# Kernel optimization log

Hardware: AMD Instinct MI355X
Metric: run time of the kernel (lower is better)

Reference implementation:

```python
import jax, jax.numpy as jnp
import numpy as np

L, D, H, N, R = 4, 256, 512, 16, 8  # layers, d_model, hidden=2*d_model, state_dim, dt_rank
OUT_LEN, IN_DIM = 96, 32
EPS = 1e-5


def _layernorm(v, g, b):
    m = jnp.mean(v, axis=-1, keepdims=True)
    var = jnp.mean((v - m) ** 2, axis=-1, keepdims=True)
    return (v - m) / jnp.sqrt(var + EPS) * g + b


def _pos_encoding(T, d):
    pos = jnp.arange(T, dtype=jnp.float32)[:, None]
    div = jnp.exp(jnp.arange(0, d, 2, dtype=jnp.float32) * (-np.log(10000.0) / d))
    pe = jnp.zeros((T, d), dtype=jnp.float32)
    pe = pe.at[:, 0::2].set(jnp.sin(pos * div))
    pe = pe.at[:, 1::2].set(jnp.cos(pos * div))
    return pe


def setup_inputs() -> dict:
    key = jax.random.key(0)
    ks = jax.random.split(key, 20)
    inp = {
        "x": jax.random.normal(ks[0], (8, 1024, IN_DIM), dtype=jnp.float32),
        "emb_w": jax.random.normal(ks[1], (D, IN_DIM), dtype=jnp.float32) * 0.1,
        "emb_b": jnp.zeros((D,), dtype=jnp.float32),
        "norm_g": jnp.ones((L, D), dtype=jnp.float32),
        "norm_b": jnp.zeros((L, D), dtype=jnp.float32),
        "in_w": jax.random.normal(ks[2], (L, H, D), dtype=jnp.float32) * (1.0 / np.sqrt(D)),
        "conv_w": jax.random.normal(ks[3], (L, H, 1, 3), dtype=jnp.float32) * 0.5,
        "A_p": jax.random.normal(ks[4], (L, H, N), dtype=jnp.float32) * 0.01,
        "D_p": jnp.ones((L, H), dtype=jnp.float32),
        "dt1_w": jax.random.normal(ks[5], (L, R, H), dtype=jnp.float32) * (1.0 / np.sqrt(H)),
        "dt1_b": jnp.zeros((L, R), dtype=jnp.float32),
        "dt2_w": jax.random.normal(ks[6], (L, H, R), dtype=jnp.float32) * (1.0 / np.sqrt(R)),
        "dt2_b": jnp.zeros((L, H), dtype=jnp.float32),
        "out_w": jax.random.normal(ks[7], (L, D, H), dtype=jnp.float32) * (1.0 / np.sqrt(H)),
        "final_g": jnp.ones((D,), dtype=jnp.float32),
        "final_b": jnp.zeros((D,), dtype=jnp.float32),
        "head1_w": jax.random.normal(ks[8], (D, D), dtype=jnp.float32) * (1.0 / np.sqrt(D)),
        "head1_b": jnp.zeros((D,), dtype=jnp.float32),
        "head2_w": jax.random.normal(ks[9], (OUT_LEN, D), dtype=jnp.float32) * (1.0 / np.sqrt(D)),
        "head2_b": jnp.zeros((OUT_LEN,), dtype=jnp.float32),
    }
    return inp


def _mamba_block(h, g, b, in_w, conv_w, A_p, D_p, dt1_w, dt1_b, dt2_w, dt2_b, out_w):
    res = h
    v = _layernorm(h, g, b)            # [B,T,D]
    v = jnp.einsum('btd,hd->bth', v, in_w)  # [B,T,H]
    # depthwise conv1d, kernel 3, padding 1, groups=H
    vc = jnp.transpose(v, (0, 2, 1))   # [B,H,T]
    vc = jax.lax.conv_general_dilated(vc, conv_w, window_strides=(1,),
                                      padding=[(1, 1)], feature_group_count=H,
                                      dimension_numbers=('NCH', 'OIH', 'NCH'))
    v = jnp.transpose(jax.nn.silu(vc), (0, 2, 1))  # [B,T,H]
    dt = jax.nn.relu(jnp.einsum('bth,rh->btr', v, dt1_w) + dt1_b)
    dt = jnp.einsum('btr,hr->bth', dt, dt2_w) + dt2_b
    dt = jax.nn.softplus(dt)           # [B,T,H]
    A = -jnp.exp(A_p)                  # [H,N]
    safe_A = jnp.where(jnp.abs(A) < 1e-5, jnp.ones_like(A), A)

    B_sz = v.shape[0]
    state0 = jnp.zeros((B_sz, H, N), dtype=v.dtype)

    def step(state, inp):
        x_t, dt_t = inp  # [B,H] each
        dA = A * dt_t[..., None]            # [B,H,N]
        discA = jnp.exp(dA)
        discB = (discA - 1.0) / safe_A * dt_t[..., None]
        state = discA * state + discB * x_t[..., None]
        y = jnp.einsum('bhn,hn->bh', state, A_p) + D_p * x_t
        return state, y

    xs = (jnp.transpose(v, (1, 0, 2)), jnp.transpose(dt, (1, 0, 2)))  # [T,B,H]
    _, ys = jax.lax.scan(step, state0, xs)
    y = jnp.transpose(ys, (1, 0, 2))   # [B,T,H]
    return res + jnp.einsum('bth,dh->btd', y, out_w)


def reference(x, emb_w, emb_b, norm_g, norm_b, in_w, conv_w, A_p, D_p,
              dt1_w, dt1_b, dt2_w, dt2_b, out_w, final_g, final_b,
              head1_w, head1_b, head2_w, head2_b):
    h = jnp.einsum('bti,di->btd', x, emb_w) + emb_b  # [B,T,D]
    h = h + _pos_encoding(h.shape[1], D)[None]
    for l in range(L):
        h = _mamba_block(h, norm_g[l], norm_b[l], in_w[l], conv_w[l], A_p[l],
                         D_p[l], dt1_w[l], dt1_b[l], dt2_w[l], dt2_b[l], out_w[l])
    h = _layernorm(h, final_g, final_b)
    h = h[:, -1, :]                    # last token [B,D]
    h = jax.nn.silu(h @ head1_w.T + head1_b)
    return h @ head2_w.T + head2_b     # [B, OUT_LEN]
```

## Files before the change

kernel.cpp:

```cpp
#include <hip/hip_runtime.h>
#include <hip/hip_bf16.h>
#include <math.h>

#define BB 8
#define TT 1024
#define DD 256
#define HH 512
#define NN 16
#define RR 8
#define OUT_LEN 96
#define IN_DIM 32
#define MM (BB*TT)

#define SC 16
#define CC (TT/SC)

typedef unsigned short u16;
typedef unsigned int u32;
typedef __attribute__((ext_vector_type(8))) short short8;
typedef __attribute__((ext_vector_type(8))) unsigned short u16x8;
typedef __attribute__((ext_vector_type(4))) float float4v;

__device__ __forceinline__ u16 f2bf(float f) {
    __hip_bfloat16 h = __float2bfloat16(f);
    return *(u16*)&h;
}
__device__ __forceinline__ float bf2f(u16 u) {
    u32 v = ((u32)u) << 16;
    return *(float*)&v;
}

#define GLD_LDS16(src, dst) __builtin_amdgcn_global_load_lds( \
    (const __attribute__((address_space(1))) void*)(src),     \
    (__attribute__((address_space(3))) void*)(dst), 16, 0, 0)

#define SBAR()   asm volatile("s_barrier" ::: "memory")
#define VMCNT0() asm volatile("s_waitcnt vmcnt(0)" ::: "memory")
#define VMCNT4() asm volatile("s_waitcnt vmcnt(4)" ::: "memory")
#define VMCNT6() asm volatile("s_waitcnt vmcnt(6)" ::: "memory")
#define VMCNT8() asm volatile("s_waitcnt vmcnt(8)" ::: "memory")

__global__ __launch_bounds__(256) void embed_ln_cvt_kernel(
    const float* __restrict__ x, const float* __restrict__ emb_w,
    const float* __restrict__ emb_b,
    const float* __restrict__ g, const float* __restrict__ b,
    float* __restrict__ h, u16* __restrict__ lnout,
    const float* __restrict__ w_in, u16* __restrict__ wbf_in,
    const float* __restrict__ w_out, u16* __restrict__ wbf_out, int nw)
{
    int bid = blockIdx.x;
    if (bid >= MM) {
        int i = (bid - MM) * 256 + threadIdx.x;
        if (i < nw) wbf_in[i] = f2bf(w_in[i]);
        else        wbf_out[i - nw] = f2bf(w_out[i - nw]);
        return;
    }

    int bt = bid;
    int d  = threadIdx.x;
    int t  = bt & (TT - 1);

    __shared__ float xs[IN_DIM];
    __shared__ float red[4], red2[4];
    if (threadIdx.x < IN_DIM) xs[threadIdx.x] = x[bt * IN_DIM + threadIdx.x];
    __syncthreads();

    const float* w = emb_w + d * IN_DIM;
    float acc = emb_b[d];
#pragma unroll
    for (int i = 0; i < IN_DIM; i++) acc = fmaf(xs[i], w[i], acc);

    int i2 = d & ~1;
    float div = __expf(-(float)i2 * 0.0359778918f);
    float arg = (float)t * div;
    float pe = (d & 1) ? __cosf(arg) : __sinf(arg);
    float val = acc + pe;
    h[bt * DD + d] = val;

    float s = val;
#pragma unroll
    for (int o = 32; o > 0; o >>= 1) s += __shfl_down(s, o);
    int lane = d & 63, wave = d >> 6;
    if (lane == 0) red[wave] = s;
    __syncthreads();
    float mean = (red[0] + red[1] + red[2] + red[3]) * (1.0f / DD);

    float c = val - mean;
    float s2 = c * c;
#pragma unroll
    for (int o = 32; o > 0; o >>= 1) s2 += __shfl_down(s2, o);
    if (lane == 0) red2[wave] = s2;
    __syncthreads();
    float var = (red2[0] + red2[1] + red2[2] + red2[3]) * (1.0f / DD);

    lnout[bt * DD + d] = f2bf(c * rsqrtf(var + 1e-5f) * g[d] + b[d]);
}

template<int BM, int BN, int OUT_BF16>
__global__ __launch_bounds__(256) void gemm_bf16(
    const u16* __restrict__ A, const u16* __restrict__ B,
    void* __restrict__ Cv, int M, int N, int K, int addC)
{
    constexpr int BK = 64;
    constexpr int MT = BM / 32;
    constexpr int NT = BN / 32;
    static_assert(BM == 128 && BN == 64, "vmcnt count assumes 6 loads/thread");

    __shared__ __align__(16) u16 Al[2][8][BM][8];
    __shared__ __align__(16) u16 Bl[2][8][BN][8];

    const int tid = threadIdx.x;
    const int bm = blockIdx.y * BM;
    const int bn = blockIdx.x * BN;
    const int wid = tid >> 6, lane = tid & 63;
    const int wm = wid >> 1, wn = wid & 1;
    const int lq = lane >> 4, lm = lane & 15;

    float4v acc[MT][NT];
#pragma unroll
    for (int i = 0; i < MT; i++)
#pragma unroll
        for (int j = 0; j < NT; j++) acc[i][j] = (float4v){0.f, 0.f, 0.f, 0.f};

#pragma unroll
    for (int it = 0; it < (8 * BM) / 256; it++) {
        int c = it * 256 + tid;
        int q = c / BM, row = c % BM;
        GLD_LDS16(A + (size_t)(bm + row) * K + q * 8, &Al[0][q][row][0]);
    }
#pragma unroll
    for (int it = 0; it < (8 * BN) / 256; it++) {
        int c = it * 256 + tid;
        int q = c / BN, row = c % BN;
        GLD_LDS16(B + (size_t)(bn + row) * K + q * 8, &Bl[0][q][row][0]);
    }

    const int nt = K / BK;
    int cur = 0;
    for (int i = 0; i < nt; i++) {
        if (i + 1 < nt) {
            int nxt = cur ^ 1;
            int k1 = (i + 1) * BK;
#pragma unroll
            for (int it = 0; it < (8 * BM) / 256; it++) {
                int c = it * 256 + tid;
                int q = c / BM, row = c % BM;
                GLD_LDS16(A + (size_t)(bm + row) * K + k1 + q * 8, &Al[nxt][q][row][0]);
            }
#pragma unroll
            for (int it = 0; it < (8 * BN) / 256; it++) {
                int c = it * 256 + tid;
                int q = c / BN, row = c % BN;
                GLD_LDS16(B + (size_t)(bn + row) * K + k1 + q * 8, &Bl[nxt][q][row][0]);
            }
            VMCNT6();
        } else {
            VMCNT0();
        }
        SBAR();

        short8 af[2][MT], bf[2][NT];
#pragma unroll
        for (int kk = 0; kk < 2; kk++) {
#pragma unroll
            for (int mt = 0; mt < MT; mt++)
                af[kk][mt] = *(const short8*)&Al[cur][kk * 4 + lq][wm * (BM / 2) + mt * 16 + lm][0];
#pragma unroll
            for (int nt2 = 0; nt2 < NT; nt2++)
                bf[kk][nt2] = *(const short8*)&Bl[cur][kk * 4 + lq][wn * (BN / 2) + nt2 * 16 + lm][0];
        }

#pragma unroll
        for (int kk = 0; kk < 2; kk++)
#pragma unroll
            for (int mt = 0; mt < MT; mt++)
#pragma unroll
                for (int nt2 = 0; nt2 < NT; nt2++)
                    acc[mt][nt2] = __builtin_amdgcn_mfma_f32_16x16x32_bf16(
                        af[kk][mt], bf[kk][nt2], acc[mt][nt2], 0, 0, 0);
        SBAR();
        cur ^= 1;
    }

#pragma unroll
    for (int mt = 0; mt < MT; mt++)
#pragma unroll
        for (int nt2 = 0; nt2 < NT; nt2++) {
            int row0 = bm + wm * (BM / 2) + mt * 16 + lq * 4;
            int col  = bn + wn * (BN / 2) + nt2 * 16 + lm;
#pragma unroll
            for (int r = 0; r < 4; r++) {
                float vv = acc[mt][nt2][r];
                if (OUT_BF16) {
                    ((u16*)Cv)[(size_t)(row0 + r) * N + col] = f2bf(vv);
                } else {
                    float* cp = (float*)Cv + (size_t)(row0 + r) * N + col;
                    if (addC) vv += *cp;
                    *cp = vv;
                }
            }
        }
}

__device__ __forceinline__ float softplus_f(float s) {
    return (s > 20.0f) ? s : __logf(1.0f + __expf(s));
}

__global__ __launch_bounds__(512, 4) void conv_scan1(
    const u16* __restrict__ vbf, const float* __restrict__ cwg,
    const float* __restrict__ w1g, const float* __restrict__ b1g,
    const float* __restrict__ dt2_w, const float* __restrict__ dt2_b,
    const float* __restrict__ A_p,
    u16* __restrict__ vsb, float* __restrict__ dtr,
    u16* __restrict__ Lst, float* __restrict__ sdt)
{
    const int c = blockIdx.x;
    const int b = blockIdx.y;
    const int tid = threadIdx.x;
    const int wave = tid >> 6, lane = tid & 63;
    const int h0 = lane * 8;

    __shared__ float w1s[RR * 2 * 256];
    __shared__ u16   a_lds[SC][HH];
    __shared__ float ds[SC * RR];

#pragma unroll
    for (int i = 0; i < 2; i++) {
        int rci = wave + i * 8;
        int r = rci >> 1, jc = rci & 1;
        float4 wv = *(const float4*)(w1g + r * HH + lane * 8 + jc * 4);
        *(float4*)&w1s[rci * 256 + lane * 4] = wv;
    }
    __syncthreads();

    const float* wp = cwg + h0 * 3;
#pragma unroll
    for (int i = 0; i < 2; i++) {
        int tr = wave + i * 8;
        int t  = c * SC + tr;
        size_t m = (size_t)b * TT + t;

        const u16* vrow = vbf + m * HH + h0;
        u16x8 x0 = *(const u16x8*)vrow;
        u16x8 xm = (t > 0)      ? *(const u16x8*)(vrow - HH) : (u16x8)(0);
        u16x8 xp = (t < TT - 1) ? *(const u16x8*)(vrow + HH) : (u16x8)(0);

        float a[8];
        u16x8 o;
#pragma unroll
        for (int j = 0; j < 8; j++) {
            float s = wp[j * 3] * bf2f(xm[j]);
            s = fmaf(wp[j * 3 + 1], bf2f(x0[j]), s);
            s = fmaf(wp[j * 3 + 2], bf2f(xp[j]), s);
            s = s / (1.0f + __expf(-s));
            a[j] = s;
            o[j] = f2bf(s);
        }
        *(u16x8*)(vsb + m * HH + h0) = o;
        *(u16x8*)&a_lds[tr][h0]      = o;

        float acc[RR];
#pragma unroll
        for (int r = 0; r < RR; r++) {
            float4 wlo = *(const float4*)&w1s[(r * 2 + 0) * 256 + lane * 4];
            float4 whi = *(const float4*)&w1s[(r * 2 + 1) * 256 + lane * 4];
            float s = a[0] * wlo.x;
            s = fmaf(a[1], wlo.y, s);
            s = fmaf(a[2], wlo.z, s);
            s = fmaf(a[3], wlo.w, s);
            s = fmaf(a[4], whi.x, s);
            s = fmaf(a[5], whi.y, s);
            s = fmaf(a[6], whi.z, s);
            s = fmaf(a[7], whi.w, s);
            acc[r] = s;
        }
#pragma unroll
        for (int r = 0; r < RR; r++) {
#pragma unroll
            for (int o2 = 1; o2 < 64; o2 <<= 1) acc[r] += __shfl_xor(acc[r], o2);
        }
        if (lane == 0) {
#pragma unroll
            for (int r = 0; r < RR; r++) acc[r] = fmaxf(acc[r] + b1g[r], 0.0f);
            *(float4*)(dtr + m * RR)     = make_float4(acc[0], acc[1], acc[2], acc[3]);
            *(float4*)(dtr + m * RR + 4) = make_float4(acc[4], acc[5], acc[6], acc[7]);
#pragma unroll
            for (int r = 0; r < RR; r++) ds[tr * RR + r] = acc[r];
        }
    }
    __syncthreads();

    const int h = tid;
    float A2[NN], invA[NN], st[NN];
    const float* ap = A_p + h * NN;
#pragma unroll
    for (int n = 0; n < NN; n++) {
        float av = -__expf(ap[n]);
        A2[n] = av * 1.44269504f;
        invA[n] = 1.0f / av;
        st[n] = 0.0f;
    }
    float w2[RR];
#pragma unroll
    for (int r = 0; r < RR; r++) w2[r] = dt2_w[h * RR + r];
    float b2 = dt2_b[h];

    float xv = bf2f(a_lds[0][h]);
    float s_dt = 0.0f;
#pragma unroll 2
    for (int t = 0; t < SC; t++) {
        float xn = (t + 1 < SC) ? bf2f(a_lds[t + 1][h]) : 0.0f;
        float s = b2;
#pragma unroll
        for (int r = 0; r < RR; r++) s = fmaf(ds[t * RR + r], w2[r], s);
        float dt = softplus_f(s);
        s_dt += dt;
        float dtx = dt * xv;
#pragma unroll
        for (int n = 0; n < NN; n++) {
            float e = __builtin_amdgcn_exp2f(A2[n] * dt);
            float u = invA[n] * dtx;
            st[n] = fmaf(e, st[n] + u, -u);
        }
        xv = xn;
    }

    size_t base = (((size_t)c * BB + b) * HH + h) * NN;
    u16x8 lo, hi;
#pragma unroll
    for (int n = 0; n < 8; n++) { lo[n] = f2bf(st[n]); hi[n] = f2bf(st[n + 8]); }
    *(u16x8*)(Lst + base)     = lo;
    *(u16x8*)(Lst + base + 8) = hi;
    sdt[((size_t)c * BB + b) * HH + h] = s_dt;
}

__global__ __launch_bounds__(256) void scan_carry_par(
    const float* __restrict__ A_p, const float* __restrict__ sdt,
    u16* __restrict__ Lst)
{
    int gw   = (blockIdx.x << 2) | (threadIdx.x >> 6);
    int lane = threadIdx.x & 63;
    int b = gw >> 9;
    int h = gw & 511;

    size_t sidx = ((size_t)lane * BB + b) * HH + h;
    float sd = sdt[sidx];
    const float* ap = A_p + h * NN;
    u16x8 Llo = *(const u16x8*)(Lst + sidx * NN);
    u16x8 Lhi = *(const u16x8*)(Lst + sidx * NN + 8);
    u16x8 Elo, Ehi;
#pragma unroll
    for (int n = 0; n < NN; n++) {
        float An = -__expf(ap[n]);
        float p  = __expf(An * sd);
        float lv = bf2f((n < 8) ? Llo[n] : Lhi[n - 8]);
#pragma unroll
        for (int d2 = 1; d2 < 64; d2 <<= 1) {
            float pp = __shfl_up(p, d2);
            float pl = __shfl_up(lv, d2);
            if (lane >= d2) { lv = fmaf(pl, p, lv); p = pp * p; }
        }
        float E = __shfl_up(lv, 1);
        if (lane == 0) E = 0.0f;
        if (n < 8) Elo[n] = f2bf(E); else Ehi[n - 8] = f2bf(E);
    }
    *(u16x8*)(Lst + sidx * NN)     = Elo;
    *(u16x8*)(Lst + sidx * NN + 8) = Ehi;
}

__global__ __launch_bounds__(512) void scan2_gemm2_ln(
    const u16* __restrict__ vsb, const float* __restrict__ dtr,
    const float* __restrict__ dt2_w, const float* __restrict__ dt2_b,
    const float* __restrict__ A_p, const float* __restrict__ D_p,
    const u16* __restrict__ carry,
    const u16* __restrict__ B,
    float* __restrict__ h,
    const float* __restrict__ g, const float* __restrict__ bb,
    u16* __restrict__ lnout, int doLN,
    const float* __restrict__ w1h, const float* __restrict__ b1h,
    const float* __restrict__ w2h, const float* __restrict__ b2h,
    float* __restrict__ outp, int doHead)
{
    const int bid = blockIdx.x;
    const int b   = bid >> 5;
    const int tb  = bid & 31;
    const int t0  = tb * 32;
    const int c0  = tb * 2;
    const int bm  = bid * 32;

    const int tid = threadIdx.x;
    const int wid = tid >> 6;
    const int lane = tid & 63;
    const int lq = lane >> 4, lm = lane & 15;
    const int wm = wid >> 2;
    const int wn = wid & 3;

    __shared__ __align__(16) u16 Yl[32 * 512];
    __shared__ __align__(16) u16 Bl[3][8][256][8];
    __shared__ float ds[32 * RR];
    __shared__ float rs[4][32], qs[4][32];
    __shared__ float hn[DD], sl1[DD];

#pragma unroll
    for (int pt = 0; pt < 2; pt++) {
#pragma unroll
        for (int it = 0; it < 4; it++) {
            int cth = it * 512 + tid;
            int q = cth >> 8, row = cth & 255;
            GLD_LDS16(B + (size_t)row * 512 + pt * 64 + q * 8, &Bl[pt][q][row][0]);
        }
    }

    if (tid < 256) {
        int tr = tid >> 3, r = tid & 7;
        ds[tid] = dtr[((size_t)b * TT + t0 + tr) * RR + r];
    }

    const int hh = tid;
    float A2[NN], invA[NN], Ap[NN], w2[RR];
    const float* ap = A_p + hh * NN;
#pragma unroll
    for (int n = 0; n < NN; n++) {
        float apv = ap[n]; Ap[n] = apv;
        float a = -__expf(apv);
        A2[n] = a * 1.44269504f; invA[n] = 1.0f / a;
    }
#pragma unroll
    for (int r = 0; r < RR; r++) w2[r] = dt2_w[hh * RR + r];
    float b2 = dt2_b[hh];
    float Dp = D_p[hh];
    __syncthreads();

#pragma unroll
    for (int cc = 0; cc < 2; cc++) {
        int cg = c0 + cc;
        float st[NN];
        size_t cbase = (((size_t)cg * BB + b) * HH + hh) * NN;
        u16x8 clo = *(const u16x8*)(carry + cbase);
        u16x8 chi = *(const u16x8*)(carry + cbase + 8);
#pragma unroll
        for (int n = 0; n < 8; n++) { st[n] = bf2f(clo[n]); st[n + 8] = bf2f(chi[n]); }

        const u16* vbase = vsb + ((size_t)b * TT + (size_t)cg * SC) * HH + hh;
        float xv = bf2f(vbase[0]);
#pragma unroll 2
        for (int t = 0; t < SC; t++) {
            float xn = (t + 1 < SC) ? bf2f(vbase[(size_t)(t + 1) * HH]) : 0.0f;
            int tr = cc * SC + t;
            float s = b2;
#pragma unroll
            for (int r = 0; r < RR; r++) s = fmaf(ds[tr * RR + r], w2[r], s);
            float dt = softplus_f(s);
            float dtx = dt * xv;
            float acc = Dp * xv;
#pragma unroll
            for (int n = 0; n < NN; n++) {
                float e = __builtin_amdgcn_exp2f(A2[n] * dt);
                float u = invA[n] * dtx;
                st[n] = fmaf(e, st[n] + u, -u);
                acc = fmaf(st[n], Ap[n], acc);
            }
            Yl[tr * 512 + (hh ^ ((tr & 7) << 3))] = f2bf(acc);
            xv = xn;
        }
    }
    __syncthreads();

    float4v acc4[4];
#pragma unroll
    for (int j = 0; j < 4; j++) acc4[j] = (float4v){0.f, 0.f, 0.f, 0.f};

    for (int i = 0; i < 8; i++) {
        if (i + 2 < 8) {
            int nb = (i + 2) % 3;
            int k1 = (i + 2) * 64;
#pragma unroll
            for (int it = 0; it < 4; it++) {
                int cth = it * 512 + tid;
                int q = cth >> 8, row = cth & 255;
                GLD_LDS16(B + (size_t)row * 512 + k1 + q * 8, &Bl[nb][q][row][0]);
            }
            VMCNT8();
        } else if (i + 1 < 8) {
            VMCNT4();
        } else {
            VMCNT0();
        }
        SBAR();

        int cur = i % 3;
        int k0 = i * 64;
        short8 af[2], bf[2][4];
#pragma unroll
        for (int kk = 0; kk < 2; kk++) {
            int row = wm * 16 + lm;
            int kg  = (k0 >> 3) + kk * 4 + lq;
            af[kk] = *(const short8*)&Yl[row * 512 + ((kg ^ (row & 7)) << 3)];
#pragma unroll
            for (int nt = 0; nt < 4; nt++)
                bf[kk][nt] = *(const short8*)&Bl[cur][kk * 4 + lq][wn * 64 + nt * 16 + lm][0];
        }
#pragma unroll
        for (int kk = 0; kk < 2; kk++)
#pragma unroll
            for (int nt = 0; nt < 4; nt++)
                acc4[nt] = __builtin_amdgcn_mfma_f32_16x16x32_bf16(
                    af[kk], bf[kk][nt], acc4[nt], 0, 0, 0);
        SBAR();
    }

    float val[4][4];
    float s1[4] = {0.f, 0.f, 0.f, 0.f}, s2[4] = {0.f, 0.f, 0.f, 0.f};
#pragma unroll
    for (int r = 0; r < 4; r++) {
        int row = bm + wm * 16 + lq * 4 + r;
#pragma unroll
        for (int nt = 0; nt < 4; nt++) {
            int col = wn * 64 + nt * 16 + lm;
            float v = acc4[nt][r] + h[(size_t)row * DD + col];
            val[r][nt] = v;
            s1[r] += v;
            s2[r] = fmaf(v, v, s2[r]);
            h[(size_t)row * DD + col] = v;
        }
    }
#pragma unroll
    for (int r = 0; r < 4; r++) {
#pragma unroll
        for (int o = 1; o < 16; o <<= 1) {
            s1[r] += __shfl_xor(s1[r], o);
            s2[r] += __shfl_xor(s2[r], o);
        }
    }
    if (lm == 0) {
#pragma unroll
        for (int r = 0; r < 4; r++) {
            rs[wn][wm * 16 + lq * 4 + r] = s1[r];
            qs[wn][wm * 16 + lq * 4 + r] = s2[r];
        }
    }
    __syncthreads();

    if (doLN) {
#pragma unroll
        for (int r = 0; r < 4; r++) {
            int i = wm * 16 + lq * 4 + r;
            int row = bm + i;
            float mean = (rs[0][i] + rs[1][i] + rs[2][i] + rs[3][i]) * (1.0f / DD);
            float var  = (qs[0][i] + qs[1][i] + qs[2][i] + qs[3][i]) * (1.0f / DD) - mean * mean;
            float rstd = rsqrtf(var + 1e-5f);
#pragma unroll
            for (int nt = 0; nt < 4; nt++) {
                int col = wn * 64 + nt * 16 + lm;
                lnout[(size_t)row * DD + col] =
                    f2bf((val[r][nt] - mean) * rstd * g[col] + bb[col]);
            }
        }
    }

    if (doHead && tb == 31) {
        const int i31 = 31;
        float mean = (rs[0][i31] + rs[1][i31] + rs[2][i31] + rs[3][i31]) * (1.0f / DD);
        float var  = (qs[0][i31] + qs[1][i31] + qs[2][i31] + qs[3][i31]) * (1.0f / DD) - mean * mean;
        float rstd = rsqrtf(var + 1e-5f);
        const size_t row = (size_t)bm + 31;

        if (tid < DD) {
            float v = h[row * DD + tid];
            hn[tid] = (v - mean) * rstd * g[tid] + bb[tid];
        }
        __syncthreads();

        if (tid < DD) {
            float a1 = b1h[tid];
            const float* w1r = w1h + tid * DD;
#pragma unroll 8
            for (int k = 0; k < DD; k++) a1 = fmaf(hn[k], w1r[k], a1);
            sl1[tid] = a1 / (1.0f + __expf(-a1));
        }
        __syncthreads();

        if (tid < OUT_LEN) {
            float a2 = b2h[tid];
            const float* w2r = w2h + tid * DD;
#pragma unroll 8
            for (int k = 0; k < DD; k++) a2 = fmaf(sl1[k], w2r[k], a2);
            outp[b * OUT_LEN + tid] = a2;
        }
    }
}

extern "C" void kernel_launch(void* const* d_in, const int* in_sizes, int n_in,
                              void* d_out, int out_size, void* d_ws, size_t ws_size,
                              hipStream_t stream)
{
    (void)in_sizes; (void)n_in; (void)out_size; (void)ws_size;

    const float* x       = (const float*)d_in[0];
    const float* emb_w   = (const float*)d_in[1];
    const float* emb_b   = (const float*)d_in[2];
    const float* norm_g  = (const float*)d_in[3];
    const float* norm_b  = (const float*)d_in[4];
    const float* in_w    = (const float*)d_in[5];
    const float* conv_w  = (const float*)d_in[6];
    const float* A_p     = (const float*)d_in[7];
    const float* D_p     = (const float*)d_in[8];
    const float* dt1_w   = (const float*)d_in[9];
    const float* dt1_b   = (const float*)d_in[10];
    const float* dt2_w   = (const float*)d_in[11];
    const float* dt2_b   = (const float*)d_in[12];
    const float* out_w   = (const float*)d_in[13];
    const float* final_g = (const float*)d_in[14];
    const float* final_b = (const float*)d_in[15];
    const float* head1_w = (const float*)d_in[16];
    const float* head1_b = (const float*)d_in[17];
    const float* head2_w = (const float*)d_in[18];
    const float* head2_b = (const float*)d_in[19];
    float* outp = (float*)d_out;

    char* ws = (char*)d_ws;
    float* h     = (float*)ws;                ws += (size_t)MM * DD * 4;
    u16*   vbf   = (u16*)ws;                  ws += (size_t)MM * HH * 2;
    u16*   vsb   = (u16*)ws;                  ws += (size_t)MM * HH * 2;
    u16*   lnbuf = (u16*)ws;                  ws += (size_t)MM * DD * 2;
    float* dtr   = (float*)ws;                ws += (size_t)MM * RR * 4;
    u16*   Lst   = (u16*)ws;                  ws += (size_t)CC * BB * HH * NN * 2;
    float* sdt   = (float*)ws;                ws += (size_t)CC * BB * HH * 4;
    u16*   wbf_in  = (u16*)ws;                ws += (size_t)4 * HH * DD * 2;
    u16*   wbf_out = (u16*)ws;                ws += (size_t)4 * DD * HH * 2;

    const int NW = 4 * HH * DD;
    embed_ln_cvt_kernel<<<MM + (2 * NW) / 256, 256, 0, stream>>>(
        x, emb_w, emb_b, norm_g, norm_b, h, lnbuf,
        in_w, wbf_in, out_w, wbf_out, NW);

    for (int l = 0; l < 4; l++) {
        gemm_bf16<128, 64, 1><<<dim3(HH / 64, MM / 128), 256, 0, stream>>>(
            lnbuf, wbf_in + (size_t)l * HH * DD, vbf, MM, HH, DD, 0);

        conv_scan1<<<dim3(CC, BB), 512, 0, stream>>>(
            vbf, conv_w + (size_t)l * HH * 3,
            dt1_w + (size_t)l * RR * HH, dt1_b + l * RR,
            dt2_w + (size_t)l * HH * RR, dt2_b + l * HH,
            A_p + (size_t)l * HH * NN,
            vsb, dtr, Lst, sdt);

        scan_carry_par<<<(BB * HH) / 4, 256, 0, stream>>>(
            A_p + (size_t)l * HH * NN, sdt, Lst);

        const float* g_next = (l < 3) ? (norm_g + (l + 1) * DD) : final_g;
        const float* b_next = (l < 3) ? (norm_b + (l + 1) * DD) : final_b;
        scan2_gemm2_ln<<<MM / 32, 512, 0, stream>>>(
            vsb, dtr, dt2_w + (size_t)l * HH * RR, dt2_b + l * HH,
            A_p + (size_t)l * HH * NN, D_p + l * HH,
            Lst, wbf_out + (size_t)l * DD * HH,
            h, g_next, b_next, lnbuf, (l < 3) ? 1 : 0,
            head1_w, head1_b, head2_w, head2_b, outp, (l == 3) ? 1 : 0);
    }
}
```

Before: 467.9 us.

## Halve scan2_gemm2_ln tile to one chunk per block and double-buffer B

Each scan2_gemm2_ln block now handles one 16-step scan chunk (16 rows) instead of two. The grid doubles to 512 blocks and each thread scans only 16 timesteps, which shortens the serial scan per block and adds more blocks to fill the GPU. The output GEMM uses 8 waves each owning 32 columns, with a K=32 double-buffered B pipeline and launch_bounds(512,4) to allow higher occupancy. In exchange, the whole out_w weight matrix is streamed into LDS twice as many times across the grid, and the per-step barriers double.

Measured after the change: 479.1 us. +2.4%, slower.

```diff
diff --git a/kernel.cpp b/kernel.cpp
--- a/kernel.cpp
+++ b/kernel.cpp
@@ -36,9 +36,8 @@
 
 #define SBAR()   asm volatile("s_barrier" ::: "memory")
 #define VMCNT0() asm volatile("s_waitcnt vmcnt(0)" ::: "memory")
-#define VMCNT4() asm volatile("s_waitcnt vmcnt(4)" ::: "memory")
+#define VMCNT2() asm volatile("s_waitcnt vmcnt(2)" ::: "memory")
 #define VMCNT6() asm volatile("s_waitcnt vmcnt(6)" ::: "memory")
-#define VMCNT8() asm volatile("s_waitcnt vmcnt(8)" ::: "memory")
 
 __global__ __launch_bounds__(256) void embed_ln_cvt_kernel(
     const float* __restrict__ x, const float* __restrict__ emb_w,
@@ -368,7 +367,7 @@
     *(u16x8*)(Lst + sidx * NN + 8) = Ehi;
 }
 
-__global__ __launch_bounds__(512) void scan2_gemm2_ln(
+__global__ __launch_bounds__(512, 4) void scan2_gemm2_ln(
     const u16* __restrict__ vsb, const float* __restrict__ dtr,
     const float* __restrict__ dt2_w, const float* __restrict__ dt2_b,
     const float* __restrict__ A_p, const float* __restrict__ D_p,
@@ -382,41 +381,45 @@
     float* __restrict__ outp, int doHead)
 {
     const int bid = blockIdx.x;
-    const int b   = bid >> 5;
-    const int tb  = bid & 31;
-    const int t0  = tb * 32;
-    const int c0  = tb * 2;
-    const int bm  = bid * 32;
+    const int b   = bid >> 6;
+    const int tb  = bid & 63;
+    const int t0  = tb * 16;
+    const int bm  = bid * 16;
 
     const int tid = threadIdx.x;
     const int wid = tid >> 6;
     const int lane = tid & 63;
     const int lq = lane >> 4, lm = lane & 15;
-    const int wm = wid >> 2;
-    const int wn = wid & 3;
-
-    __shared__ __align__(16) u16 Yl[32 * 512];
-    __shared__ __align__(16) u16 Bl[3][8][256][8];
-    __shared__ float ds[32 * RR];
-    __shared__ float rs[4][32], qs[4][32];
+
+    __shared__ __align__(16) u16 Yl[16 * 512];
+    __shared__ __align__(16) u16 Bl[2][4][256][8];
+    __shared__ float ds[SC * RR];
+    __shared__ float rs[8][16], qs[8][16];
     __shared__ float hn[DD], sl1[DD];
 
 #pragma unroll
-    for (int pt = 0; pt < 2; pt++) {
-#pragma unroll
-        for (int it = 0; it < 4; it++) {
-            int cth = it * 512 + tid;
-            int q = cth >> 8, row = cth & 255;
-            GLD_LDS16(B + (size_t)row * 512 + pt * 64 + q * 8, &Bl[pt][q][row][0]);
-        }
-    }
-
-    if (tid < 256) {
+    for (int it = 0; it < 2; it++) {
+        int cth = it * 512 + tid;
+        int q = cth >> 8, row = cth & 255;
+        GLD_LDS16(B + (size_t)row * 512 + q * 8, &Bl[0][q][row][0]);
+    }
+
+    if (tid < SC * RR) {
         int tr = tid >> 3, r = tid & 7;
         ds[tid] = dtr[((size_t)b * TT + t0 + tr) * RR + r];
     }
 
     const int hh = tid;
+
+    float st[NN];
+    {
+        size_t cb = (((size_t)tb * BB + b) * HH + hh) * NN;
+        u16x8 lo = *(const u16x8*)(carry + cb);
+        u16x8 hi = *(const u16x8*)(carry + cb + 8);
+#pragma unroll
+        for (int n = 0; n < 8; n++) { st[n] = bf2f(lo[n]); st[n + 8] = bf2f(hi[n]); }
+    }
+
     float A2[NN], invA[NN], Ap[NN], w2[RR];
     const float* ap = A_p + hh * NN;
 #pragma unroll
@@ -431,92 +434,69 @@
     float Dp = D_p[hh];
     __syncthreads();
 
-#pragma unroll
-    for (int cc = 0; cc < 2; cc++) {
-        int cg = c0 + cc;
-        float st[NN];
-        size_t cbase = (((size_t)cg * BB + b) * HH + hh) * NN;
-        u16x8 clo = *(const u16x8*)(carry + cbase);
-        u16x8 chi = *(const u16x8*)(carry + cbase + 8);
-#pragma unroll
-        for (int n = 0; n < 8; n++) { st[n] = bf2f(clo[n]); st[n + 8] = bf2f(chi[n]); }
-
-        const u16* vbase = vsb + ((size_t)b * TT + (size_t)cg * SC) * HH + hh;
-        float xv = bf2f(vbase[0]);
+    const u16* vbase = vsb + ((size_t)b * TT + t0) * HH + hh;
+    float xv = bf2f(vbase[0]);
 #pragma unroll 2
-        for (int t = 0; t < SC; t++) {
-            float xn = (t + 1 < SC) ? bf2f(vbase[(size_t)(t + 1) * HH]) : 0.0f;
-            int tr = cc * SC + t;
-            float s = b2;
-#pragma unroll
-            for (int r = 0; r < RR; r++) s = fmaf(ds[tr * RR + r], w2[r], s);
-            float dt = softplus_f(s);
-            float dtx = dt * xv;
-            float acc = Dp * xv;
-#pragma unroll
-            for (int n = 0; n < NN; n++) {
-                float e = __builtin_amdgcn_exp2f(A2[n] * dt);
-                float u = invA[n] * dtx;
-                st[n] = fmaf(e, st[n] + u, -u);
-                acc = fmaf(st[n], Ap[n], acc);
-            }
-            Yl[tr * 512 + (hh ^ ((tr & 7) << 3))] = f2bf(acc);
-            xv = xn;
-        }
-    }
-    __syncthreads();
-
-    float4v acc4[4];
-#pragma unroll
-    for (int j = 0; j < 4; j++) acc4[j] = (float4v){0.f, 0.f, 0.f, 0.f};
-
-    for (int i = 0; i < 8; i++) {
-        if (i + 2 < 8) {
-            int nb = (i + 2) % 3;
-            int k1 = (i + 2) * 64;
-#pragma unroll
-            for (int it = 0; it < 4; it++) {
+    for (int t = 0; t < SC; t++) {
+        float xn = (t + 1 < SC) ? bf2f(vbase[(size_t)(t + 1) * HH]) : 0.0f;
+        float s = b2;
+#pragma unroll
+        for (int r = 0; r < RR; r++) s = fmaf(ds[t * RR + r], w2[r], s);
+        float dt = softplus_f(s);
+        float dtx = dt * xv;
+        float acc = Dp * xv;
+#pragma unroll
+        for (int n = 0; n < NN; n++) {
+            float e = __builtin_amdgcn_exp2f(A2[n] * dt);
+            float u = invA[n] * dtx;
+            st[n] = fmaf(e, st[n] + u, -u);
+            acc = fmaf(st[n], Ap[n], acc);
+        }
+        Yl[t * 512 + (hh ^ ((t & 7) << 3))] = f2bf(acc);
+        xv = xn;
+    }
+    __syncthreads();
+
+    float4v acc4[2];
+    acc4[0] = (float4v){0.f, 0.f, 0.f, 0.f};
+    acc4[1] = (float4v){0.f, 0.f, 0.f, 0.f};
+
+    int cur = 0;
+    for (int i = 0; i < 16; i++) {
+        if (i + 1 < 16) {
+            int nxt = cur ^ 1;
+            int k1 = (i + 1) * 32;
+#pragma unroll
+            for (int it = 0; it < 2; it++) {
                 int cth = it * 512 + tid;
                 int q = cth >> 8, row = cth & 255;
-                GLD_LDS16(B + (size_t)row * 512 + k1 + q * 8, &Bl[nb][q][row][0]);
+                GLD_LDS16(B + (size_t)row * 512 + k1 + q * 8, &Bl[nxt][q][row][0]);
             }
-            VMCNT8();
-        } else if (i + 1 < 8) {
-            VMCNT4();
+            VMCNT2();
         } else {
             VMCNT0();
         }
         SBAR();
 
-        int cur = i % 3;
-        int k0 = i * 64;
-        short8 af[2], bf[2][4];
-#pragma unroll
-        for (int kk = 0; kk < 2; kk++) {
-            int row = wm * 16 + lm;
-            int kg  = (k0 >> 3) + kk * 4 + lq;
-            af[kk] = *(const short8*)&Yl[row * 512 + ((kg ^ (row & 7)) << 3)];
-#pragma unroll
-            for (int nt = 0; nt < 4; nt++)
-                bf[kk][nt] = *(const short8*)&Bl[cur][kk * 4 + lq][wn * 64 + nt * 16 + lm][0];
-        }
-#pragma unroll
-        for (int kk = 0; kk < 2; kk++)
-#pragma unroll
-            for (int nt = 0; nt < 4; nt++)
-                acc4[nt] = __builtin_amdgcn_mfma_f32_16x16x32_bf16(
-                    af[kk], bf[kk][nt], acc4[nt], 0, 0, 0);
+        int row = lm;
+        int kg  = i * 4 + lq;
+        short8 af = *(const short8*)&Yl[row * 512 + ((kg ^ (row & 7)) << 3)];
+        short8 bf0 = *(const short8*)&Bl[cur][lq][wid * 32 + lm][0];
+        short8 bf1 = *(const short8*)&Bl[cur][lq][wid * 32 + 16 + lm][0];
+        acc4[0] = __builtin_amdgcn_mfma_f32_16x16x32_bf16(af, bf0, acc4[0], 0, 0, 0);
+        acc4[1] = __builtin_amdgcn_mfma_f32_16x16x32_bf16(af, bf1, acc4[1], 0, 0, 0);
         SBAR();
-    }
-
-    float val[4][4];
+        cur ^= 1;
+    }
+
+    float val[4][2];
     float s1[4] = {0.f, 0.f, 0.f, 0.f}, s2[4] = {0.f, 0.f, 0.f, 0.f};
 #pragma unroll
     for (int r = 0; r < 4; r++) {
-        int row = bm + wm * 16 + lq * 4 + r;
-#pragma unroll
-        for (int nt = 0; nt < 4; nt++) {
-            int col = wn * 64 + nt * 16 + lm;
+        int row = bm + lq * 4 + r;
+#pragma unroll
+        for (int nt = 0; nt < 2; nt++) {
+            int col = wid * 32 + nt * 16 + lm;
             float v = acc4[nt][r] + h[(size_t)row * DD + col];
             val[r][nt] = v;
             s1[r] += v;
@@ -535,8 +515,8 @@
     if (lm == 0) {
 #pragma unroll
         for (int r = 0; r < 4; r++) {
-            rs[wn][wm * 16 + lq * 4 + r] = s1[r];
-            qs[wn][wm * 16 + lq * 4 + r] = s2[r];
+            rs[wid][lq * 4 + r] = s1[r];
+            qs[wid][lq * 4 + r] = s2[r];
         }
     }
     __syncthreads();
@@ -544,26 +524,34 @@
     if (doLN) {
 #pragma unroll
         for (int r = 0; r < 4; r++) {
-            int i = wm * 16 + lq * 4 + r;
+            int i = lq * 4 + r;
             int row = bm + i;
-            float mean = (rs[0][i] + rs[1][i] + rs[2][i] + rs[3][i]) * (1.0f / DD);
-            float var  = (qs[0][i] + qs[1][i] + qs[2][i] + qs[3][i]) * (1.0f / DD) - mean * mean;
+            float sm = rs[0][i] + rs[1][i] + rs[2][i] + rs[3][i]
+                     + rs[4][i] + rs[5][i] + rs[6][i] + rs[7][i];
+            float sq = qs[0][i] + qs[1][i] + qs[2][i] + qs[3][i]
+                     + qs[4][i] + qs[5][i] + qs[6][i] + qs[7][i];
+            float mean = sm * (1.0f / DD);
+            float var  = sq * (1.0f / DD) - mean * mean;
             float rstd = rsqrtf(var + 1e-5f);
 #pragma unroll
-            for (int nt = 0; nt < 4; nt++) {
-                int col = wn * 64 + nt * 16 + lm;
+            for (int nt = 0; nt < 2; nt++) {
+                int col = wid * 32 + nt * 16 + lm;
                 lnout[(size_t)row * DD + col] =
                     f2bf((val[r][nt] - mean) * rstd * g[col] + bb[col]);
             }
         }
     }
 
-    if (doHead && tb == 31) {
-        const int i31 = 31;
-        float mean = (rs[0][i31] + rs[1][i31] + rs[2][i31] + rs[3][i31]) * (1.0f / DD);
-        float var  = (qs[0][i31] + qs[1][i31] + qs[2][i31] + qs[3][i31]) * (1.0f / DD) - mean * mean;
+    if (doHead && tb == 63) {
+        const int i15 = 15;
+        float sm = rs[0][i15] + rs[1][i15] + rs[2][i15] + rs[3][i15]
+                 + rs[4][i15] + rs[5][i15] + rs[6][i15] + rs[7][i15];
+        float sq = qs[0][i15] + qs[1][i15] + qs[2][i15] + qs[3][i15]
+                 + qs[4][i15] + qs[5][i15] + qs[6][i15] + qs[7][i15];
+        float mean = sm * (1.0f / DD);
+        float var  = sq * (1.0f / DD) - mean * mean;
         float rstd = rsqrtf(var + 1e-5f);
-        const size_t row = (size_t)bm + 31;
+        const size_t row = (size_t)bm + 15;
 
         if (tid < DD) {
             float v = h[row * DD + tid];
@@ -650,7 +638,7 @@
 
         const float* g_next = (l < 3) ? (norm_g + (l + 1) * DD) : final_g;
         const float* b_next = (l < 3) ? (norm_b + (l + 1) * DD) : final_b;
-        scan2_gemm2_ln<<<MM / 32, 512, 0, stream>>>(
+        scan2_gemm2_ln<<<MM / 16, 512, 0, stream>>>(
             vsb, dtr, dt2_w + (size_t)l * HH * RR, dt2_b + l * HH,
             A_p + (size_t)l * HH * NN, D_p + l * HH,
             Lst, wbf_out + (size_t)l * DD * HH,
```
